# Kernel tuning notes

Hardware: AMD Instinct MI355X
Metric: run time of the kernel (lower is better)

## Reference

```python
import jax, jax.numpy as jnp
import numpy as np

N, D_IN, D_OUT = 8192, 1024, 1024

def setup_inputs() -> dict:
    key = jax.random.key(0)
    kx, kq, kk, kv = jax.random.split(key, 4)
    s = 1.0 / np.sqrt(D_IN)
    return {
        "x": jax.random.normal(kx, (N, D_IN), dtype=jnp.float32),
        "Wq": jax.random.uniform(kq, (D_OUT, D_IN), dtype=jnp.float32, minval=-s, maxval=s),
        "Wk": jax.random.uniform(kk, (D_OUT, D_IN), dtype=jnp.float32, minval=-s, maxval=s),
        "Wv": jax.random.uniform(kv, (D_OUT, D_IN), dtype=jnp.float32, minval=-s, maxval=s),
    }

def reference(x, Wq, Wk, Wv):
    # Linear layers: y = x @ W.T (no bias, qkv_bias=False)
    q = x @ Wq.T  # [N, d_out]
    k = x @ Wk.T
    v = x @ Wv.T
    scores = q @ k.T  # [N, N]
    weights = jax.nn.softmax(scores / jnp.sqrt(jnp.float32(k.shape[-1])), axis=-1)
    return weights @ v  # [N, d_out]
```

## Files before the change

### kernel.cpp

```cpp
#include <hip/hip_runtime.h>
#include <stdint.h>

typedef __bf16 bf16_t;
typedef __bf16 bf16x8 __attribute__((ext_vector_type(8)));
typedef float f32x4 __attribute__((ext_vector_type(4)));
typedef int i32x4 __attribute__((ext_vector_type(4)));
typedef int i32x8 __attribute__((ext_vector_type(8)));

typedef const __attribute__((address_space(1))) void gv_t;
typedef __attribute__((address_space(3))) void lv_t;


template <int LDK>
__device__ __forceinline__ void stage_half2(const bf16_t* g, bf16_t* lh,
                                            int wave, int lane) {
#pragma unroll
  for (int i = 0; i < 2; ++i) {
    const int ub = i * 8192 + wave * 1024;
    const int o = ub + lane * 16;
    const int row = o >> 7;
    const int kb = (o & 127) ^ ((row & 7) << 4);
    const char* src = (const char*)g + (size_t)row * (LDK * 2) + kb;
    __builtin_amdgcn_global_load_lds((gv_t*)src, (lv_t*)(lh + (ub >> 1)), 16, 0, 0);
  }
}

__device__ __forceinline__ bf16x8 ld_frag2(const bf16_t* h, int r, int s, int lane) {
  int byte = r * 128 + s * 64 + ((lane >> 4) << 4);
  byte ^= (r & 7) << 4;
  return *(const bf16x8*)((const char*)h + byte);
}

template <int EPI, int MM, int NN, int KEXT, int LDK, int NKS>
__global__ __launch_bounds__(512) void gemm8p(
    const bf16_t* __restrict__ A, const bf16_t* __restrict__ Bt,
    float* __restrict__ Cf0, bf16_t* __restrict__ Cf1b,
    const float* __restrict__ rvec,
    uint8_t* __restrict__ qo, uint8_t* __restrict__ ko,
    bf16_t* __restrict__ vtb) {
  __shared__ __align__(16) bf16_t L[2][4][8192];

  const int tid = threadIdx.x;
  const int wave = tid >> 6;
  const int lane = tid & 63;

  const int bid = blockIdx.x;
  const int x = bid & 7;
  const int j = bid >> 3;
  int tm, tn, ks;
  if (NKS > 1) {
    ks = j >> 4;
    tm = (x << 2) | (j & 3);
    tn = (j >> 2) & 3;
  } else {
    ks = 0;
    tm = (x << 2) | (j & 3);
    tn = j >> 2;
  }

  const bf16_t* Ab = A + (size_t)tm * (256 * LDK) + (size_t)ks * KEXT;
  const bf16_t* Bb = Bt + (size_t)tn * (256 * LDK) + (size_t)ks * KEXT;

  const int wr64 = (wave >> 2) * 64;
  const int wc32 = (wave & 3) * 32;
  const int fr = lane & 15;
  constexpr int nt = KEXT >> 6;

  f32x4 acc00[4][2], acc01[4][2], acc10[4][2], acc11[4][2];
#pragma unroll
  for (int m = 0; m < 4; ++m)
#pragma unroll
    for (int n = 0; n < 2; ++n) {
      acc00[m][n] = (f32x4){0.f, 0.f, 0.f, 0.f};
      acc01[m][n] = (f32x4){0.f, 0.f, 0.f, 0.f};
      acc10[m][n] = (f32x4){0.f, 0.f, 0.f, 0.f};
      acc11[m][n] = (f32x4){0.f, 0.f, 0.f, 0.f};
    }

  stage_half2<LDK>(Ab, &L[0][0][0], wave, lane);
  stage_half2<LDK>(Ab + (size_t)128 * LDK, &L[0][1][0], wave, lane);
  stage_half2<LDK>(Bb, &L[0][2][0], wave, lane);
  stage_half2<LDK>(Bb + (size_t)128 * LDK, &L[0][3][0], wave, lane);
  stage_half2<LDK>(Ab + 64, &L[1][0][0], wave, lane);
  stage_half2<LDK>(Bb + (size_t)128 * LDK + 64, &L[1][3][0], wave, lane);
  asm volatile("s_waitcnt vmcnt(4)" ::: "memory");
  __builtin_amdgcn_s_barrier();

  bf16x8 a[4][2], bA[2][2], bB[2][2];

#pragma unroll 1
  for (int t = 0; t < nt; ++t) {
    const int cur = t & 1;
    const bf16_t* A0h = &L[cur][0][0];
    const bf16_t* A1h = &L[cur][1][0];
    const bf16_t* B0h = &L[cur][2][0];
    const bf16_t* B1h = &L[cur][3][0];

#pragma unroll
    for (int m = 0; m < 4; ++m)
#pragma unroll
      for (int s = 0; s < 2; ++s)
        a[m][s] = ld_frag2(A0h, wr64 + m * 16 + fr, s, lane);
#pragma unroll
    for (int n = 0; n < 2; ++n)
#pragma unroll
      for (int s = 0; s < 2; ++s)
        bA[n][s] = ld_frag2(B0h, wc32 + n * 16 + fr, s, lane);
    if (t + 1 < nt)
      stage_half2<LDK>(Ab + (size_t)128 * LDK + (t + 1) * 64, &L[cur ^ 1][1][0],
                       wave, lane);
    __builtin_amdgcn_s_barrier();
    __builtin_amdgcn_s_setprio(1);
#pragma unroll
    for (int s = 0; s < 2; ++s)
#pragma unroll
      for (int m = 0; m < 4; ++m)
#pragma unroll
        for (int n = 0; n < 2; ++n)
          acc00[m][n] = __builtin_amdgcn_mfma_f32_16x16x32_bf16(a[m][s], bA[n][s],
                                                                acc00[m][n], 0, 0, 0);
    __builtin_amdgcn_s_setprio(0);
    __builtin_amdgcn_s_barrier();

#pragma unroll
    for (int n = 0; n < 2; ++n)
#pragma unroll
      for (int s = 0; s < 2; ++s)
        bB[n][s] = ld_frag2(B1h, wc32 + n * 16 + fr, s, lane);
    if (t + 1 < nt)
      stage_half2<LDK>(Bb + (t + 1) * 64, &L[cur ^ 1][2][0], wave, lane);
    __builtin_amdgcn_s_barrier();
    __builtin_amdgcn_s_setprio(1);
#pragma unroll
    for (int s = 0; s < 2; ++s)
#pragma unroll
      for (int m = 0; m < 4; ++m)
#pragma unroll
        for (int n = 0; n < 2; ++n)
          acc01[m][n] = __builtin_amdgcn_mfma_f32_16x16x32_bf16(a[m][s], bB[n][s],
                                                                acc01[m][n], 0, 0, 0);
    __builtin_amdgcn_s_setprio(0);
    __builtin_amdgcn_s_barrier();

#pragma unroll
    for (int m = 0; m < 4; ++m)
#pragma unroll
      for (int s = 0; s < 2; ++s)
        a[m][s] = ld_frag2(A1h, wr64 + m * 16 + fr, s, lane);
    if (t + 2 < nt)
      stage_half2<LDK>(Ab + (t + 2) * 64, &L[cur][0][0], wave, lane);
    __builtin_amdgcn_s_barrier();
    __builtin_amdgcn_s_setprio(1);
#pragma unroll
    for (int s = 0; s < 2; ++s)
#pragma unroll
      for (int m = 0; m < 4; ++m)
#pragma unroll
        for (int n = 0; n < 2; ++n)
          acc11[m][n] = __builtin_amdgcn_mfma_f32_16x16x32_bf16(a[m][s], bB[n][s],
                                                                acc11[m][n], 0, 0, 0);
    __builtin_amdgcn_s_setprio(0);
    __builtin_amdgcn_s_barrier();

    if (t + 2 < nt)
      stage_half2<LDK>(Bb + (size_t)128 * LDK + (t + 2) * 64, &L[cur][3][0],
                       wave, lane);
    __builtin_amdgcn_s_barrier();
    __builtin_amdgcn_s_setprio(1);
#pragma unroll
    for (int s = 0; s < 2; ++s)
#pragma unroll
      for (int m = 0; m < 4; ++m)
#pragma unroll
        for (int n = 0; n < 2; ++n)
          acc10[m][n] = __builtin_amdgcn_mfma_f32_16x16x32_bf16(a[m][s], bA[n][s],
                                                                acc10[m][n], 0, 0, 0);
    __builtin_amdgcn_s_setprio(0);
    if (t + 2 < nt)
      asm volatile("s_waitcnt vmcnt(4)" ::: "memory");
    else
      asm volatile("s_waitcnt vmcnt(0)" ::: "memory");
    __builtin_amdgcn_s_barrier();
  }

  const int fro = (lane >> 4) * 4;
#define STORE_QUAD(ACC, QM, QN)                                                  \
  _Pragma("unroll") for (int m = 0; m < 4; ++m) {                                \
    _Pragma("unroll") for (int n = 0; n < 2; ++n) {                              \
      const int row = tm * 256 + QM * 128 + wr64 + m * 16 + fro;                 \
      const int col = tn * 256 + QN * 128 + wc32 + n * 16 + fr;                  \
      if (EPI == 0) {                                                            \
        const float4 rv = *(const float4*)&rvec[row];                            \
        if (ks == 0) {                                                           \
          _Pragma("unroll") for (int jj = 0; jj < 4; ++jj)                       \
              Cf0[(size_t)(row + jj) * NN + col] =                               \
                  ACC[m][n][jj] * ((const float*)&rv)[jj];                       \
        } else {                                                                 \
          _Pragma("unroll") for (int jj = 0; jj < 4; ++jj)                       \
              Cf1b[(size_t)(row + jj) * NN + col] =                              \
                  (bf16_t)(ACC[m][n][jj] * ((const float*)&rv)[jj]);             \
        }                                                                        \
      } else {                                                                   \
        if (col < 1024) {                                                        \
          _Pragma("unroll") for (int jj = 0; jj < 4; ++jj) {                     \
            int pk = __builtin_amdgcn_cvt_pk_fp8_f32(ACC[m][n][jj],              \
                                                     ACC[m][n][jj], 0, false);   \
            qo[(size_t)(row + jj) * 1024 + col] = (uint8_t)pk;                   \
          }                                                                      \
        } else if (col < 2048) {                                                 \
          _Pragma("unroll") for (int jj = 0; jj < 4; ++jj) {                     \
            int pk = __builtin_amdgcn_cvt_pk_fp8_f32(ACC[m][n][jj],              \
                                                     ACC[m][n][jj], 0, false);   \
            ko[(size_t)(row + jj) * 1024 + (col - 1024)] = (uint8_t)pk;          \
          }                                                                      \
        } else {                                                                 \
          union { bf16_t h[4]; uint2 u; } tpk;                                   \
          _Pragma("unroll") for (int jj = 0; jj < 4; ++jj)                       \
              tpk.h[jj] = (bf16_t)ACC[m][n][jj];                                 \
          *(uint2*)&vtb[(size_t)(col - 2048) * MM + row] = tpk.u;                \
        }                                                                        \
      }                                                                          \
    }                                                                            \
  }
  STORE_QUAD(acc00, 0, 0)
  STORE_QUAD(acc01, 0, 1)
  STORE_QUAD(acc10, 1, 0)
  STORE_QUAD(acc11, 1, 1)
#undef STORE_QUAD
}


__device__ __forceinline__ void stage_fp8(const uint8_t* g, uint8_t* l,
                                          int wave, int lane) {
#pragma unroll
  for (int i = 0; i < 4; ++i) {
    const int ub = i * 4096 + wave * 1024;
    const int o = ub + lane * 16;
    const int row = o >> 7;
    const int col = (o & 127) ^ ((row & 7) << 4);
    __builtin_amdgcn_global_load_lds((gv_t*)(g + (size_t)row * 1024 + col),
                                     (lv_t*)(l + ub), 16, 0, 0);
  }
}

__device__ __forceinline__ i32x8 ld_frag8(const uint8_t* base128, int row, int kg) {
  const int sw = (row & 7) << 4;
  const uint8_t* b = base128 + row * 128;
  i32x4 lo = *(const i32x4*)(b + (kg ^ sw));
  i32x4 hi = *(const i32x4*)(b + ((kg | 16) ^ sw));
  i32x8 v;
  v[0] = lo[0]; v[1] = lo[1]; v[2] = lo[2]; v[3] = lo[3];
  v[4] = hi[0]; v[5] = hi[1]; v[6] = hi[2]; v[7] = hi[3];
  return v;
}

__global__ __launch_bounds__(256) void scores_fp8(
    const uint8_t* __restrict__ qf, const uint8_t* __restrict__ kf,
    bf16_t* __restrict__ S, float* __restrict__ partial) {
  __shared__ __align__(16) uint8_t lA[2][128 * 128];
  __shared__ __align__(16) uint8_t lB[2][128 * 128];

  const int tid = threadIdx.x;
  const int wave = tid >> 6;
  const int lane = tid & 63;

  const int bid = blockIdx.x;
  const int x = bid & 7;
  const int j = bid >> 3;
  const int tm = (x << 3) | (j & 7);
  const int tn = j >> 3;

  const uint8_t* Ab = qf + (size_t)tm * 128 * 1024;
  const uint8_t* Bb = kf + (size_t)tn * 128 * 1024;

  const int wr = (wave >> 1) * 64;
  const int wc = (wave & 1) * 64;
  const int fr = lane & 15;
  const int kg = (lane >> 4) * 32;

  f32x4 acc[4][4];
#pragma unroll
  for (int m = 0; m < 4; ++m)
#pragma unroll
    for (int n = 0; n < 4; ++n) acc[m][n] = (f32x4){0.f, 0.f, 0.f, 0.f};

  stage_fp8(Ab, lA[0], wave, lane);
  stage_fp8(Bb, lB[0], wave, lane);
  __syncthreads();

#pragma unroll 1
  for (int kt = 0; kt < 8; ++kt) {
    const int cur = kt & 1;
    if (kt < 7) {
      stage_fp8(Ab + (kt + 1) * 128, lA[cur ^ 1], wave, lane);
      stage_fp8(Bb + (kt + 1) * 128, lB[cur ^ 1], wave, lane);
    }
    i32x8 a[4], b[4];
#pragma unroll
    for (int m = 0; m < 4; ++m) a[m] = ld_frag8(lA[cur], wr + m * 16 + fr, kg);
#pragma unroll
    for (int n = 0; n < 4; ++n) b[n] = ld_frag8(lB[cur], wc + n * 16 + fr, kg);
#pragma unroll
    for (int m = 0; m < 4; ++m)
#pragma unroll
      for (int n = 0; n < 4; ++n)
        acc[m][n] = __builtin_amdgcn_mfma_scale_f32_16x16x128_f8f6f4(
            a[m], b[n], acc[m][n], 0, 0, 0, 0x7F7F7F7F, 0, 0x7F7F7F7F);
    __syncthreads();
  }

  const int fro = (lane >> 4) * 4;
  float* lsum = (float*)&lA[0][0];
#pragma unroll
  for (int m = 0; m < 4; ++m) {
#pragma unroll
    for (int jj = 0; jj < 4; ++jj) {
      const int rl = wr + m * 16 + fro + jj;
      float s = 0.f;
#pragma unroll
      for (int n = 0; n < 4; ++n) {
        float e = __expf(acc[m][n][jj]);
        const int col = tn * 128 + wc + n * 16 + fr;
        S[(size_t)(tm * 128 + rl) * 8192 + col] = (bf16_t)e;
        s += e;
      }
      s += __shfl_xor(s, 1, 64);
      s += __shfl_xor(s, 2, 64);
      s += __shfl_xor(s, 4, 64);
      s += __shfl_xor(s, 8, 64);
      if (fr == 0) lsum[rl * 2 + (wave & 1)] = s;
    }
  }
  __syncthreads();
  if (tid < 128)
    partial[(size_t)tn * 8192 + tm * 128 + tid] = lsum[tid * 2] + lsum[tid * 2 + 1];
}

__global__ __launch_bounds__(256) void cvt_f32_bf16(const float* __restrict__ s,
                                                    bf16_t* __restrict__ d,
                                                    int n8, float scale) {
  int i = blockIdx.x * 256 + threadIdx.x;
  if (i >= n8) return;
  const float4* sp = (const float4*)s + (size_t)i * 2;
  float4 x0 = sp[0], x1 = sp[1];
  bf16x8 o;
  o[0] = (bf16_t)(x0.x * scale);
  o[1] = (bf16_t)(x0.y * scale);
  o[2] = (bf16_t)(x0.z * scale);
  o[3] = (bf16_t)(x0.w * scale);
  o[4] = (bf16_t)(x1.x * scale);
  o[5] = (bf16_t)(x1.y * scale);
  o[6] = (bf16_t)(x1.z * scale);
  o[7] = (bf16_t)(x1.w * scale);
  ((bf16x8*)d)[i] = o;
}

__global__ __launch_bounds__(256) void rowsum_recip(const float* __restrict__ partial,
                                                    float* __restrict__ r) {
  int row = blockIdx.x * 256 + threadIdx.x;
  float s = 0.f;
#pragma unroll
  for (int t = 0; t < 64; ++t) s += partial[(size_t)t * 8192 + row];
  r[row] = 1.0f / s;
}

__global__ __launch_bounds__(256) void add_p1(float* __restrict__ out,
                                              const bf16_t* __restrict__ p1b) {
  size_t i = (size_t)blockIdx.x * 256 + threadIdx.x;
  bf16x8 b = ((const bf16x8*)p1b)[i];
  float4 a0 = ((const float4*)out)[i * 2];
  float4 a1 = ((const float4*)out)[i * 2 + 1];
  a0.x += (float)b[0];
  a0.y += (float)b[1];
  a0.z += (float)b[2];
  a0.w += (float)b[3];
  a1.x += (float)b[4];
  a1.y += (float)b[5];
  a1.z += (float)b[6];
  a1.w += (float)b[7];
  ((float4*)out)[i * 2] = a0;
  ((float4*)out)[i * 2 + 1] = a1;
}

extern "C" void kernel_launch(void* const* d_in, const int* in_sizes, int n_in,
                              void* d_out, int out_size, void* d_ws, size_t ws_size,
                              hipStream_t stream) {
  const int N = 8192, D = 1024;
  const float* x = (const float*)d_in[0];
  const float* Wq = (const float*)d_in[1];
  const float* Wk = (const float*)d_in[2];
  const float* Wv = (const float*)d_in[3];
  float* out = (float*)d_out;

  uint8_t* qf = (uint8_t*)d_ws;
  uint8_t* kf = qf + (size_t)N * D;
  bf16_t* vt = (bf16_t*)(kf + (size_t)N * D);
  bf16_t* S = vt + (size_t)N * D;
  bf16_t* xb = S;
  bf16_t* Wb = xb + (size_t)N * D;
  bf16_t* P1b = (bf16_t*)d_ws;
  float* rvec = (float*)(S + (size_t)N * N);
  float* partial = out;

  const float sq = 0.1767766953f;

  cvt_f32_bf16<<<(N * D / 8) / 256, 256, 0, stream>>>(x, xb, N * D / 8, 1.0f);
  cvt_f32_bf16<<<(D * D / 8) / 256, 256, 0, stream>>>(Wq, Wb, D * D / 8, sq);
  cvt_f32_bf16<<<(D * D / 8) / 256, 256, 0, stream>>>(Wk, Wb + (size_t)D * D,
                                                      D * D / 8, sq);
  cvt_f32_bf16<<<(D * D / 8) / 256, 256, 0, stream>>>(Wv, Wb + (size_t)2 * D * D,
                                                      D * D / 8, 1.0f);

  gemm8p<2, 8192, 3072, 1024, 1024, 1><<<(N / 256) * (3 * D / 256), 512, 0, stream>>>(
      xb, Wb, nullptr, nullptr, nullptr, qf, kf, vt);

  scores_fp8<<<(N / 128) * (N / 128), 256, 0, stream>>>(qf, kf, S, partial);

  rowsum_recip<<<N / 256, 256, 0, stream>>>(partial, rvec);

  gemm8p<0, 8192, 1024, 4096, 8192, 2><<<(N / 256) * (D / 256) * 2, 512, 0, stream>>>(
      S, vt, out, P1b, rvec, nullptr, nullptr, nullptr);

  add_p1<<<(N * D / 8) / 256, 256, 0, stream>>>(out, P1b);
}
```

Measured before the change: 330.4 us.

## Restructure FP8 scores kernel into 256x256 tiles with 8-wave ping-pong pipeline

Rewrites the QK^T scores kernel to compute 256x256 output tiles with 512 threads, splitting LDS into four 128-row half-tiles that are staged asynchronously and interleaved with MFMA quadrants under barriers and s_setprio. It mirrors the pipelined structure of the existing gemm8p kernel. The goal is to raise arithmetic intensity per byte loaded and overlap global-to-LDS loads with matrix compute. The rowsum reduction now sums over 32 column tiles instead of 64. Larger tiles cut the grid to 1024 blocks and raise register pressure.

```diff
diff --git a/kernel.cpp b/kernel.cpp
--- a/kernel.cpp
+++ b/kernel.cpp
@@ -230,35 +230,35 @@
 }
 
 
-__device__ __forceinline__ void stage_fp8(const uint8_t* g, uint8_t* l,
-                                          int wave, int lane) {
-#pragma unroll
-  for (int i = 0; i < 4; ++i) {
-    const int ub = i * 4096 + wave * 1024;
+__device__ __forceinline__ void stage_half8(const uint8_t* g, uint8_t* lh,
+                                            int wave, int lane) {
+#pragma unroll
+  for (int i = 0; i < 2; ++i) {
+    const int ub = i * 8192 + wave * 1024;
     const int o = ub + lane * 16;
     const int row = o >> 7;
     const int col = (o & 127) ^ ((row & 7) << 4);
     __builtin_amdgcn_global_load_lds((gv_t*)(g + (size_t)row * 1024 + col),
-                                     (lv_t*)(l + ub), 16, 0, 0);
-  }
-}
-
-__device__ __forceinline__ i32x8 ld_frag8(const uint8_t* base128, int row, int kg) {
-  const int sw = (row & 7) << 4;
-  const uint8_t* b = base128 + row * 128;
+                                     (lv_t*)(lh + ub), 16, 0, 0);
+  }
+}
+
+__device__ __forceinline__ i32x8 ld_frag8h(const uint8_t* h, int r, int lane) {
+  const int sw = (r & 7) << 4;
+  const int kg = (lane >> 4) * 32;
+  const uint8_t* b = h + r * 128;
   i32x4 lo = *(const i32x4*)(b + (kg ^ sw));
-  i32x4 hi = *(const i32x4*)(b + ((kg | 16) ^ sw));
+  i32x4 hi = *(const i32x4*)(b + ((kg ^ sw) ^ 16));
   i32x8 v;
   v[0] = lo[0]; v[1] = lo[1]; v[2] = lo[2]; v[3] = lo[3];
   v[4] = hi[0]; v[5] = hi[1]; v[6] = hi[2]; v[7] = hi[3];
   return v;
 }
 
-__global__ __launch_bounds__(256) void scores_fp8(
+__global__ __launch_bounds__(512) void scores8p(
     const uint8_t* __restrict__ qf, const uint8_t* __restrict__ kf,
     bf16_t* __restrict__ S, float* __restrict__ partial) {
-  __shared__ __align__(16) uint8_t lA[2][128 * 128];
-  __shared__ __align__(16) uint8_t lB[2][128 * 128];
+  __shared__ __align__(16) uint8_t L[2][4][16384];
 
   const int tid = threadIdx.x;
   const int wave = tid >> 6;
@@ -267,73 +267,154 @@
   const int bid = blockIdx.x;
   const int x = bid & 7;
   const int j = bid >> 3;
-  const int tm = (x << 3) | (j & 7);
-  const int tn = j >> 3;
-
-  const uint8_t* Ab = qf + (size_t)tm * 128 * 1024;
-  const uint8_t* Bb = kf + (size_t)tn * 128 * 1024;
-
-  const int wr = (wave >> 1) * 64;
-  const int wc = (wave & 1) * 64;
+  const int tm = (x << 2) | (j & 3);
+  const int tn = j >> 2;
+
+  const uint8_t* Ab = qf + (size_t)tm * 256 * 1024;
+  const uint8_t* Bb = kf + (size_t)tn * 256 * 1024;
+
+  const int wr64 = (wave >> 2) * 64;
+  const int wc32 = (wave & 3) * 32;
   const int fr = lane & 15;
-  const int kg = (lane >> 4) * 32;
-
-  f32x4 acc[4][4];
+  constexpr int nt = 8;
+
+  f32x4 acc00[4][2], acc01[4][2], acc10[4][2], acc11[4][2];
 #pragma unroll
   for (int m = 0; m < 4; ++m)
 #pragma unroll
-    for (int n = 0; n < 4; ++n) acc[m][n] = (f32x4){0.f, 0.f, 0.f, 0.f};
-
-  stage_fp8(Ab, lA[0], wave, lane);
-  stage_fp8(Bb, lB[0], wave, lane);
+    for (int n = 0; n < 2; ++n) {
+      acc00[m][n] = (f32x4){0.f, 0.f, 0.f, 0.f};
+      acc01[m][n] = (f32x4){0.f, 0.f, 0.f, 0.f};
+      acc10[m][n] = (f32x4){0.f, 0.f, 0.f, 0.f};
+      acc11[m][n] = (f32x4){0.f, 0.f, 0.f, 0.f};
+    }
+
+  stage_half8(Ab, &L[0][0][0], wave, lane);
+  stage_half8(Ab + (size_t)128 * 1024, &L[0][1][0], wave, lane);
+  stage_half8(Bb, &L[0][2][0], wave, lane);
+  stage_half8(Bb + (size_t)128 * 1024, &L[0][3][0], wave, lane);
+  stage_half8(Ab + 128, &L[1][0][0], wave, lane);
+  stage_half8(Bb + (size_t)128 * 1024 + 128, &L[1][3][0], wave, lane);
+  asm volatile("s_waitcnt vmcnt(4)" ::: "memory");
+  __builtin_amdgcn_s_barrier();
+
+  i32x8 a[4], bA[2], bB[2];
+
+#pragma unroll 1
+  for (int t = 0; t < nt; ++t) {
+    const int cur = t & 1;
+    const uint8_t* A0h = &L[cur][0][0];
+    const uint8_t* A1h = &L[cur][1][0];
+    const uint8_t* B0h = &L[cur][2][0];
+    const uint8_t* B1h = &L[cur][3][0];
+
+#pragma unroll
+    for (int m = 0; m < 4; ++m) a[m] = ld_frag8h(A0h, wr64 + m * 16 + fr, lane);
+#pragma unroll
+    for (int n = 0; n < 2; ++n) bA[n] = ld_frag8h(B0h, wc32 + n * 16 + fr, lane);
+    if (t + 1 < nt)
+      stage_half8(Ab + (size_t)128 * 1024 + (t + 1) * 128, &L[cur ^ 1][1][0],
+                  wave, lane);
+    __builtin_amdgcn_s_barrier();
+    __builtin_amdgcn_s_setprio(1);
+#pragma unroll
+    for (int m = 0; m < 4; ++m)
+#pragma unroll
+      for (int n = 0; n < 2; ++n)
+        acc00[m][n] = __builtin_amdgcn_mfma_scale_f32_16x16x128_f8f6f4(
+            a[m], bA[n], acc00[m][n], 0, 0, 0, 0x7F7F7F7F, 0, 0x7F7F7F7F);
+    __builtin_amdgcn_s_setprio(0);
+    __builtin_amdgcn_s_barrier();
+
+#pragma unroll
+    for (int n = 0; n < 2; ++n) bB[n] = ld_frag8h(B1h, wc32 + n * 16 + fr, lane);
+    if (t + 1 < nt)
+      stage_half8(Bb + (t + 1) * 128, &L[cur ^ 1][2][0], wave, lane);
+    __builtin_amdgcn_s_barrier();
+    __builtin_amdgcn_s_setprio(1);
+#pragma unroll
+    for (int m = 0; m < 4; ++m)
+#pragma unroll
+      for (int n = 0; n < 2; ++n)
+        acc01[m][n] = __builtin_amdgcn_mfma_scale_f32_16x16x128_f8f6f4(
+            a[m], bB[n], acc01[m][n], 0, 0, 0, 0x7F7F7F7F, 0, 0x7F7F7F7F);
+    __builtin_amdgcn_s_setprio(0);
+    __builtin_amdgcn_s_barrier();
+
+#pragma unroll
+    for (int m = 0; m < 4; ++m) a[m] = ld_frag8h(A1h, wr64 + m * 16 + fr, lane);
+    if (t + 2 < nt)
+      stage_half8(Ab + (t + 2) * 128, &L[cur][0][0], wave, lane);
+    __builtin_amdgcn_s_barrier();
+    __builtin_amdgcn_s_setprio(1);
+#pragma unroll
+    for (int m = 0; m < 4; ++m)
+#pragma unroll
+      for (int n = 0; n < 2; ++n)
+        acc11[m][n] = __builtin_amdgcn_mfma_scale_f32_16x16x128_f8f6f4(
+            a[m], bB[n], acc11[m][n], 0, 0, 0, 0x7F7F7F7F, 0, 0x7F7F7F7F);
+    __builtin_amdgcn_s_setprio(0);
+    __builtin_amdgcn_s_barrier();
+
+    if (t + 2 < nt)
+      stage_half8(Bb + (size_t)128 * 1024 + (t + 2) * 128, &L[cur][3][0],
+                  wave, lane);
+    __builtin_amdgcn_s_barrier();
+    __builtin_amdgcn_s_setprio(1);
+#pragma unroll
+    for (int m = 0; m < 4; ++m)
+#pragma unroll
+      for (int n = 0; n < 2; ++n)
+        acc10[m][n] = __builtin_amdgcn_mfma_scale_f32_16x16x128_f8f6f4(
+            a[m], bA[n], acc10[m][n], 0, 0, 0, 0x7F7F7F7F, 0, 0x7F7F7F7F);
+    __builtin_amdgcn_s_setprio(0);
+    if (t + 2 < nt)
+      asm volatile("s_waitcnt vmcnt(4)" ::: "memory");
+    else
+      asm volatile("s_waitcnt vmcnt(0)" ::: "memory");
+    __builtin_amdgcn_s_barrier();
+  }
+
+  const int fro = (lane >> 4) * 4;
+#define EXPSTORE(ACC, QM, QN)                                                    \
+  _Pragma("unroll") for (int m = 0; m < 4; ++m)                                  \
+  _Pragma("unroll") for (int n = 0; n < 2; ++n)                                  \
+  _Pragma("unroll") for (int jj = 0; jj < 4; ++jj) {                             \
+    float e = __expf(ACC[m][n][jj]);                                             \
+    ACC[m][n][jj] = e;                                                           \
+    const int row = tm * 256 + QM * 128 + wr64 + m * 16 + fro + jj;              \
+    const int col = tn * 256 + QN * 128 + wc32 + n * 16 + fr;                    \
+    S[(size_t)row * 8192 + col] = (bf16_t)e;                                     \
+  }
+  EXPSTORE(acc00, 0, 0)
+  EXPSTORE(acc01, 0, 1)
+  EXPSTORE(acc10, 1, 0)
+  EXPSTORE(acc11, 1, 1)
+#undef EXPSTORE
+  float* lsum = (float*)&L[0][0][0];
+#define ROWSUM(A0, A1, QM)                                                       \
+  _Pragma("unroll") for (int m = 0; m < 4; ++m) {                                \
+    _Pragma("unroll") for (int jj = 0; jj < 4; ++jj) {                           \
+      float s = A0[m][0][jj] + A0[m][1][jj] + A1[m][0][jj] + A1[m][1][jj];       \
+      s += __shfl_xor(s, 1, 64);                                                 \
+      s += __shfl_xor(s, 2, 64);                                                 \
+      s += __shfl_xor(s, 4, 64);                                                 \
+      s += __shfl_xor(s, 8, 64);                                                 \
+      if (fr == 0) {                                                             \
+        const int rl = QM * 128 + wr64 + m * 16 + fro + jj;                      \
+        lsum[rl * 4 + (wave & 3)] = s;                                           \
+      }                                                                          \
+    }                                                                            \
+  }
+  ROWSUM(acc00, acc01, 0)
+  ROWSUM(acc10, acc11, 1)
+#undef ROWSUM
   __syncthreads();
-
-#pragma unroll 1
-  for (int kt = 0; kt < 8; ++kt) {
-    const int cur = kt & 1;
-    if (kt < 7) {
-      stage_fp8(Ab + (kt + 1) * 128, lA[cur ^ 1], wave, lane);
-      stage_fp8(Bb + (kt + 1) * 128, lB[cur ^ 1], wave, lane);
-    }
-    i32x8 a[4], b[4];
-#pragma unroll
-    for (int m = 0; m < 4; ++m) a[m] = ld_frag8(lA[cur], wr + m * 16 + fr, kg);
-#pragma unroll
-    for (int n = 0; n < 4; ++n) b[n] = ld_frag8(lB[cur], wc + n * 16 + fr, kg);
-#pragma unroll
-    for (int m = 0; m < 4; ++m)
-#pragma unroll
-      for (int n = 0; n < 4; ++n)
-        acc[m][n] = __builtin_amdgcn_mfma_scale_f32_16x16x128_f8f6f4(
-            a[m], b[n], acc[m][n], 0, 0, 0, 0x7F7F7F7F, 0, 0x7F7F7F7F);
-    __syncthreads();
-  }
-
-  const int fro = (lane >> 4) * 4;
-  float* lsum = (float*)&lA[0][0];
-#pragma unroll
-  for (int m = 0; m < 4; ++m) {
-#pragma unroll
-    for (int jj = 0; jj < 4; ++jj) {
-      const int rl = wr + m * 16 + fro + jj;
-      float s = 0.f;
-#pragma unroll
-      for (int n = 0; n < 4; ++n) {
-        float e = __expf(acc[m][n][jj]);
-        const int col = tn * 128 + wc + n * 16 + fr;
-        S[(size_t)(tm * 128 + rl) * 8192 + col] = (bf16_t)e;
-        s += e;
-      }
-      s += __shfl_xor(s, 1, 64);
-      s += __shfl_xor(s, 2, 64);
-      s += __shfl_xor(s, 4, 64);
-      s += __shfl_xor(s, 8, 64);
-      if (fr == 0) lsum[rl * 2 + (wave & 1)] = s;
-    }
-  }
-  __syncthreads();
-  if (tid < 128)
-    partial[(size_t)tn * 8192 + tm * 128 + tid] = lsum[tid * 2] + lsum[tid * 2 + 1];
+  if (tid < 256) {
+    float s = lsum[tid * 4] + lsum[tid * 4 + 1] + lsum[tid * 4 + 2] +
+              lsum[tid * 4 + 3];
+    partial[(size_t)tn * 8192 + tm * 256 + tid] = s;
+  }
 }
 
 __global__ __launch_bounds__(256) void cvt_f32_bf16(const float* __restrict__ s,
@@ -360,7 +441,7 @@
   int row = blockIdx.x * 256 + threadIdx.x;
   float s = 0.f;
 #pragma unroll
-  for (int t = 0; t < 64; ++t) s += partial[(size_t)t * 8192 + row];
+  for (int t = 0; t < 32; ++t) s += partial[(size_t)t * 8192 + row];
   r[row] = 1.0f / s;
 }
 
@@ -414,7 +495,7 @@
   gemm8p<2, 8192, 3072, 1024, 1024, 1><<<(N / 256) * (3 * D / 256), 512, 0, stream>>>(
       xb, Wb, nullptr, nullptr, nullptr, qf, kf, vt);
 
-  scores_fp8<<<(N / 128) * (N / 128), 256, 0, stream>>>(qf, kf, S, partial);
+  scores8p<<<(N / 256) * (N / 256), 512, 0, stream>>>(qf, kf, S, partial);
 
   rowsum_recip<<<N / 256, 256, 0, stream>>>(partial, rvec);
 
```

Result: faster. 314.3 us (-4.9%).
